# Kernel optimization log

Measured on AMD Instinct MI355X. Metric: run time of the kernel, lower is better.

The kernel has to match this reference:

```python
import jax, jax.numpy as jnp
import numpy as np

B, F_IN, HID, H, S = 256, 1024, 1024, 16, 128
TEMP = float((HID // H) ** 0.5)  # 8.0


def setup_inputs() -> dict:
    key = jax.random.key(0)
    ks = jax.random.split(key, 7)
    return {
        "x": jax.random.normal(ks[0], (B, F_IN, S), dtype=jnp.float32),
        "Wq": jax.random.normal(ks[1], (HID, F_IN), dtype=jnp.float32) * (1.0 / np.sqrt(F_IN)),
        "bq": jax.random.normal(ks[2], (HID,), dtype=jnp.float32) * 0.01,
        "Wk": jax.random.normal(ks[3], (HID, F_IN), dtype=jnp.float32) * (1.0 / np.sqrt(F_IN)),
        "bk": jax.random.normal(ks[4], (HID,), dtype=jnp.float32) * 0.01,
        "Wo": jax.random.normal(ks[5], (S,), dtype=jnp.float32) * (1.0 / np.sqrt(S)),
        "bo": jax.random.normal(ks[6], (1,), dtype=jnp.float32) * 0.01,
    }


def _to_heads(t):
    # (B, F, S) -> (B, H, S, F//H), matching reshape(B,H,F/H,S).permute(0,1,3,2)
    b, f, s = t.shape
    return t.reshape(b, H, f // H, s).transpose(0, 1, 3, 2)


def reference(x, Wq, bq, Wk, bk, Wo, bo):
    # 1x1 Conv1d == per-position linear over channel dim
    q = jnp.einsum('bis,hi->bhs', x, Wq) + bq[None, :, None]
    k = jnp.einsum('bis,hi->bhs', x, Wk) + bk[None, :, None]
    qh = _to_heads(q)          # (B,H,S,HID/H)
    kh = _to_heads(k)          # (B,H,S,HID/H)
    vh = _to_heads(x)          # (B,H,S,F_IN/H)  -- v is the raw input, unprojected
    scores = jnp.einsum('bhsd,bhtd->bhst', qh, kh) / TEMP
    attn = jax.nn.softmax(scores, axis=-1)
    out = jnp.einsum('bhst,bhtd->bhsd', attn, vh)   # (B,H,S,F_IN/H)
    # _reshape_from_batches: (B,H,S,dv) -> (B, F_IN, S)
    out = out.transpose(0, 1, 3, 2).reshape(x.shape[0], F_IN, S)
    # map_o: Linear(num_users, 1) over last axis, then squeeze
    score = jnp.einsum('bfs,s->bf', out, Wo) + bo[0]
    return score
```

## Files before the change

### kernel.cpp

```cpp
#include <hip/hip_runtime.h>

#define F 1024
#define S 128
#define H 16
#define D 64
#define CK 64
#define NCHUNK 16

typedef short bf16x8 __attribute__((ext_vector_type(8)));
typedef float f32x4  __attribute__((ext_vector_type(4)));

#define XS_UNITS ((size_t)128 * NCHUNK * 2048)
#define WB_UNITS ((size_t)8 * NCHUNK * 2048)
#define WS_NEED ((XS_UNITS + WB_UNITS) * 16)

#define MAIN_LDS_BYTES (8192 * 16 + 8 * 128 * 4 + 128 * 4)

__device__ __forceinline__ unsigned short f2bf(float f) {
    unsigned u = __float_as_uint(f);
    u += 0x7fffu + ((u >> 16) & 1u);
    return (unsigned short)(u >> 16);
}

__device__ __forceinline__ uint4 pack8(const float* f) {
    uint4 u;
    u.x = (unsigned)f2bf(f[0]) | ((unsigned)f2bf(f[1]) << 16);
    u.y = (unsigned)f2bf(f[2]) | ((unsigned)f2bf(f[3]) << 16);
    u.z = (unsigned)f2bf(f[4]) | ((unsigned)f2bf(f[5]) << 16);
    u.w = (unsigned)f2bf(f[6]) | ((unsigned)f2bf(f[7]) << 16);
    return u;
}

typedef __attribute__((address_space(1))) const unsigned int as1_u32;
typedef __attribute__((address_space(3))) unsigned int as3_u32;

__device__ __forceinline__ void async_cp16(const uint4* g, uint4* l) {
    __builtin_amdgcn_global_load_lds((as1_u32*)g, (as3_u32*)l, 16, 0, 0);
}

__device__ __forceinline__ void bar()   { asm volatile("s_barrier" ::: "memory"); }
__device__ __forceinline__ void lgkm0() { asm volatile("s_waitcnt lgkmcnt(0)" ::: "memory"); }

template<int N> __device__ __forceinline__ void vmcnt_wait() {
    if constexpr (N == 8)      asm volatile("s_waitcnt vmcnt(8)" ::: "memory");
    else if constexpr (N == 4) asm volatile("s_waitcnt vmcnt(4)" ::: "memory");
    else                       asm volatile("s_waitcnt vmcnt(0)" ::: "memory");
}

__global__ void prep(const float* __restrict__ x,
                     const float* __restrict__ Wq,
                     const float* __restrict__ Wk,
                     uint4* __restrict__ xs,
                     uint4* __restrict__ wb)
{
    __shared__ float tile[64 * 129];
    const int tid = threadIdx.x;
    const int blk = blockIdx.x;
    if (blk < 4096) {
        const int b = blk >> 4, ch = blk & 15;
        const float4* src = (const float4*)(x + ((size_t)b * F + ch * CK) * S);
        float4 v[8];
#pragma unroll
        for (int j = 0; j < 8; ++j) v[j] = src[tid + j * 256];
#pragma unroll
        for (int j = 0; j < 8; ++j) {
            const int e4 = tid + j * 256;
            const int i  = e4 >> 5;
            const int sc = (e4 & 31) * 4;
            tile[i * 129 + sc + 0] = v[j].x;
            tile[i * 129 + sc + 1] = v[j].y;
            tile[i * 129 + sc + 2] = v[j].z;
            tile[i * 129 + sc + 3] = v[j].w;
        }
        __syncthreads();
        uint4* dst = xs + ((size_t)(b >> 1) * NCHUNK + ch) * 2048 + (b & 1) * 128;
#pragma unroll
        for (int j = 0; j < 4; ++j) {
            const int u  = tid + j * 256;
            const int kc = u >> 7;
            const int s  = u & 127;
            float f[8];
#pragma unroll
            for (int jj = 0; jj < 8; ++jj) f[jj] = tile[(kc * 8 + jj) * 129 + s];
            dst[kc * 256 + s] = pack8(f);
        }
    } else {
        const int blk2 = blk - 4096;
        const int h = blk2 >> 4, ch = blk2 & 15;
        uint4* dst = wb + ((size_t)(h >> 1) * NCHUNK + ch) * 2048 + (h & 1) * 128;
#pragma unroll
        for (int j = 0; j < 4; ++j) {
            const int u  = tid + j * 256;
            const int kc = u >> 7;
            const int m  = u & 127;
            const float* srcp = (m < 64)
                ? (Wq + (size_t)(h * D + m) * F + ch * CK + kc * 8)
                : (Wk + (size_t)(h * D + m - 64) * F + ch * CK + kc * 8);
            float f[8];
            float4 a = ((const float4*)srcp)[0];
            float4 c = ((const float4*)srcp)[1];
            f[0] = a.x; f[1] = a.y; f[2] = a.z; f[3] = a.w;
            f[4] = c.x; f[5] = c.y; f[6] = c.z; f[7] = c.w;
            dst[kc * 256 + m] = pack8(f);
        }
    }
}

__device__ __forceinline__ void read4(const uint4* mat, int base, bf16x8 (&r)[4]) {
    r[0] = *(const bf16x8*)&mat[base];
    r[1] = *(const bf16x8*)&mat[base + 16];
    r[2] = *(const bf16x8*)&mat[base + 32];
    r[3] = *(const bf16x8*)&mat[base + 48];
}

template<int RB>
__device__ __forceinline__ void mfma16(f32x4 (&acc)[8][4], const bf16x8 (&af)[4], const bf16x8 (&br)[4]) {
#pragma unroll
    for (int mt = 0; mt < 4; ++mt)
#pragma unroll
        for (int nt = 0; nt < 4; ++nt)
            acc[RB + mt][nt] = __builtin_amdgcn_mfma_f32_16x16x32_bf16(af[mt], br[nt], acc[RB + mt][nt], 0, 0, 0);
}

template<int HALF>
__device__ __forceinline__ void stage_half(uint4* mat, const uint4* wbase, const uint4* xbase,
                                           int tgt, int wv, int lane) {
    const int bufb = (tgt & 1) * 4096;
    const uint4* g;
    int l;
    if constexpr (HALF == 0)      { g = wbase + (size_t)tgt * 2048;        l = bufb;        }
    else if constexpr (HALF == 1) { g = xbase + (size_t)tgt * 2048;        l = bufb + 2048; }
    else if constexpr (HALF == 2) { g = wbase + (size_t)tgt * 2048 + 1024; l = bufb + 1024; }
    else                          { g = xbase + (size_t)tgt * 2048 + 1024; l = bufb + 3072; }
    async_cp16(g + wv * 128 + lane,      &mat[l + wv * 128]);
    async_cp16(g + wv * 128 + 64 + lane, &mat[l + wv * 128 + 64]);
}

template<int CUR, bool I1, bool I2, int W1, int W2, bool DW2>
__device__ __forceinline__ void ktile(uint4* mat, const uint4* wbase, const uint4* xbase,
                                      int t, int wv, int lane, int wm, int wn, int q, int l15,
                                      f32x4 (&acc)[8][4])
{
    bf16x8 af[4], br[4];
    const int abase = CUR * 4096 + wm * 128 + l15;
    const int bbase = CUR * 4096 + 2048 + wn * 64 + l15;
    const int kq = q * 256;
    read4(mat, abase + kq, af);
    read4(mat, bbase + kq, br);
    if constexpr (I1) stage_half<2>(mat, wbase, xbase, t + 1, wv, lane);
    bar(); lgkm0();
    __builtin_amdgcn_s_setprio(1); mfma16<0>(acc, af, br); __builtin_amdgcn_s_setprio(0);
    bar();
    read4(mat, abase + kq + 64, af);
    if constexpr (I1) stage_half<3>(mat, wbase, xbase, t + 1, wv, lane);
    bar(); lgkm0();
    __builtin_amdgcn_s_setprio(1); mfma16<4>(acc, af, br); __builtin_amdgcn_s_setprio(0);
    vmcnt_wait<W1>(); bar();
    read4(mat, abase + kq + 1024, af);
    read4(mat, bbase + kq + 1024, br);
    if constexpr (I2) stage_half<0>(mat, wbase, xbase, t + 2, wv, lane);
    bar(); lgkm0();
    __builtin_amdgcn_s_setprio(1); mfma16<0>(acc, af, br); __builtin_amdgcn_s_setprio(0);
    bar();
    read4(mat, abase + kq + 1024 + 64, af);
    if constexpr (I2) stage_half<1>(mat, wbase, xbase, t + 2, wv, lane);
    bar(); lgkm0();
    __builtin_amdgcn_s_setprio(1); mfma16<4>(acc, af, br); __builtin_amdgcn_s_setprio(0);
    if constexpr (DW2) { vmcnt_wait<W2>(); bar(); }
}

__launch_bounds__(512, 2)
__global__ void attn_main(const float* __restrict__ x,
                          const uint4* __restrict__ xs,
                          const uint4* __restrict__ wb,
                          const float* __restrict__ bq,
                          const float* __restrict__ bk,
                          const float* __restrict__ Wo,
                          const float* __restrict__ bo,
                          float* __restrict__ out)
{
    extern __shared__ char smraw[];
    uint4* mat   = (uint4*)smraw;
    float* wpart = (float*)(smraw + 8192 * 16);
    float* wfin  = wpart + 8 * 128;

    const int tid  = threadIdx.x;
    const int lane = tid & 63;
    const int wv   = tid >> 6;
    const int l15  = lane & 15;
    const int q    = lane >> 4;
    const int wm   = wv >> 2;
    const int wn   = wv & 3;

    const int g    = blockIdx.x;
    const int xcd  = g & 7;
    const int slot = g >> 3;
    const int bg   = xcd * 16 + (slot & 15);
    const int hg   = slot >> 4;

    const uint4* wbase = wb + (size_t)hg * NCHUNK * 2048;
    const uint4* xbase = xs + (size_t)bg * NCHUNK * 2048;

    f32x4 acc[8][4];
#pragma unroll
    for (int mi = 0; mi < 8; ++mi)
#pragma unroll
        for (int ni = 0; ni < 4; ++ni) acc[mi][ni] = (f32x4){0.f, 0.f, 0.f, 0.f};

    stage_half<0>(mat, wbase, xbase, 0, wv, lane);
    stage_half<1>(mat, wbase, xbase, 0, wv, lane);
    stage_half<2>(mat, wbase, xbase, 0, wv, lane);
    stage_half<3>(mat, wbase, xbase, 0, wv, lane);
    stage_half<0>(mat, wbase, xbase, 1, wv, lane);
    stage_half<1>(mat, wbase, xbase, 1, wv, lane);
    vmcnt_wait<8>();
    bar();

#pragma unroll 1
    for (int i = 0; i < 7; ++i) {
        ktile<0, true, true, 8, 8, true>(mat, wbase, xbase, 2 * i,     wv, lane, wm, wn, q, l15, acc);
        ktile<1, true, true, 8, 8, true>(mat, wbase, xbase, 2 * i + 1, wv, lane, wm, wn, q, l15, acc);
    }
    ktile<0, true,  false, 8, 4, true >(mat, wbase, xbase, 14, wv, lane, wm, wn, q, l15, acc);
    ktile<1, false, false, 0, 0, false>(mat, wbase, xbase, 15, wv, lane, wm, wn, q, l15, acc);

    __syncthreads();

    {
        unsigned short* m16 = (unsigned short*)mat;
        const int hglob = hg * 2 + wm;
#pragma unroll
        for (int rt = 0; rt < 8; ++rt) {
            const int mh0   = rt * 16 + q * 4;
            const int d0    = mh0 & 63;
            const int kbase = (mh0 < 64) ? 0 : 1024;
            float bias4[4];
#pragma unroll
            for (int rr = 0; rr < 4; ++rr)
                bias4[rr] = (mh0 < 64) ? bq[hglob * D + d0 + rr] : bk[hglob * D + d0 + rr];
#pragma unroll
            for (int ct = 0; ct < 4; ++ct) {
                const int col = wn * 64 + ct * 16 + l15;
                const int bj  = col >> 7;
                const int s   = col & 127;
                const int c   = wm * 2 + bj;
                unsigned long long pv = 0;
#pragma unroll
                for (int rr = 0; rr < 4; ++rr)
                    pv |= (unsigned long long)f2bf(acc[rt][ct][rr] + bias4[rr]) << (16 * rr);
                const int unit = c * 2048 + kbase + s * 8 + ((d0 >> 3) ^ (s & 7));
                *(unsigned long long*)&m16[unit * 8 + (d0 & 7)] = pv;
            }
        }
    }
    __syncthreads();

    for (int c = 0; c < 4; ++c) {
        const int qb = c * 2048;
        const int kb = c * 2048 + 1024;
        f32x4 p[8];
#pragma unroll
        for (int nt = 0; nt < 8; ++nt) p[nt] = (f32x4){0.f, 0.f, 0.f, 0.f};
#pragma unroll
        for (int ks = 0; ks < 2; ++ks) {
            const int kcq  = ks * 4 + q;
            const int arow = wv * 16 + l15;
            bf16x8 a2 = *(const bf16x8*)&mat[qb + arow * 8 + (kcq ^ (arow & 7))];
            bf16x8 b2[8];
#pragma unroll
            for (int nt = 0; nt < 8; ++nt) {
                const int trow = nt * 16 + l15;
                b2[nt] = *(const bf16x8*)&mat[kb + trow * 8 + (kcq ^ (trow & 7))];
            }
#pragma unroll
            for (int nt = 0; nt < 8; ++nt)
                p[nt] = __builtin_amdgcn_mfma_f32_16x16x32_bf16(a2, b2[nt], p[nt], 0, 0, 0);
        }
        float pw[8];
#pragma unroll
        for (int nt = 0; nt < 8; ++nt) pw[nt] = 0.f;
#pragma unroll
        for (int rr = 0; rr < 4; ++rr) {
            const int srow = wv * 16 + q * 4 + rr;
            float mx = p[0][rr];
#pragma unroll
            for (int nt = 1; nt < 8; ++nt) mx = fmaxf(mx, p[nt][rr]);
#pragma unroll
            for (int off = 1; off < 16; off <<= 1) mx = fmaxf(mx, __shfl_xor(mx, off));
            float e[8];
            float l = 0.f;
#pragma unroll
            for (int nt = 0; nt < 8; ++nt) {
                e[nt] = __expf((p[nt][rr] - mx) * 0.125f);
                l += e[nt];
            }
#pragma unroll
            for (int off = 1; off < 16; off <<= 1) l += __shfl_xor(l, off);
            const float cw = Wo[srow] / l;
#pragma unroll
            for (int nt = 0; nt < 8; ++nt) pw[nt] = fmaf(cw, e[nt], pw[nt]);
        }
#pragma unroll
        for (int nt = 0; nt < 8; ++nt) {
            pw[nt] += __shfl_xor(pw[nt], 16);
            pw[nt] += __shfl_xor(pw[nt], 32);
        }
        if (q == 0) {
#pragma unroll
            for (int nt = 0; nt < 8; ++nt) wpart[wv * 128 + nt * 16 + l15] = pw[nt];
        }
        __syncthreads();
        if (tid < 128) {
            float sum = 0.f;
#pragma unroll
            for (int w = 0; w < 8; ++w) sum += wpart[w * 128 + tid];
            wfin[tid] = sum;
        }
        __syncthreads();
        {
            const int bglob = bg * 2 + (c & 1);
            const int hglob = hg * 2 + (c >> 1);
            const int dd = tid >> 3, part = tid & 7;
            const float4* xv = (const float4*)(x + (size_t)bglob * (F * S)
                                                 + (size_t)(hglob * D + dd) * S + part * 16);
            float a5 = 0.f;
#pragma unroll
            for (int j = 0; j < 4; ++j) {
                float4 vv = xv[j];
                a5 = fmaf(wfin[part * 16 + j * 4 + 0], vv.x, a5);
                a5 = fmaf(wfin[part * 16 + j * 4 + 1], vv.y, a5);
                a5 = fmaf(wfin[part * 16 + j * 4 + 2], vv.z, a5);
                a5 = fmaf(wfin[part * 16 + j * 4 + 3], vv.w, a5);
            }
            a5 += __shfl_xor(a5, 1);
            a5 += __shfl_xor(a5, 2);
            a5 += __shfl_xor(a5, 4);
            if (part == 0) out[(size_t)bglob * F + hglob * D + dd] = a5 + bo[0];
        }
        __syncthreads();
    }
}

struct SmemT {
    uint4 mat[2048];
    float wpart[4][S];
    float wfin[S];
};

__launch_bounds__(256, 4)
__global__ void attn_fallback(const float* __restrict__ x,
                              const float* __restrict__ Wq,
                              const float* __restrict__ bq,
                              const float* __restrict__ Wk,
                              const float* __restrict__ bk,
                              const float* __restrict__ Wo,
                              const float* __restrict__ bo,
                              float* __restrict__ out)
{
    __shared__ SmemT sm;
    const int tid  = threadIdx.x;
    const int lane = tid & 63;
    const int wv   = tid >> 6;
    const int l15  = lane & 15;
    const int q    = lane >> 4;

    const int g    = blockIdx.x;
    const int xcd  = g & 7;
    const int slot = g >> 3;
    const int hg   = slot >> 7;
    const int r0   = slot & 127;
    const int b    = xcd * 32 + (r0 >> 2);
    const int h    = hg * 4 + (r0 & 3);

    const float* xb  = x  + (size_t)b * (F * S);
    const float* wqh = Wq + (size_t)h * D * F;
    const float* wkh = Wk + (size_t)h * D * F;

    const int m0 = (wv & 1) * 64;
    const int n0 = (wv >> 1) * 64;

    f32x4 acc[4][4];
#pragma unroll
    for (int mt = 0; mt < 4; ++mt)
#pragma unroll
        for (int nt = 0; nt < 4; ++nt) acc[mt][nt] = (f32x4){0.f, 0.f, 0.f, 0.f};

    const int mq  = tid >> 2;
    const int kq  = tid & 3;
    const int s0x = (tid & 63) * 2;
    const int iq  = tid >> 6;

    for (int ch = 0; ch < NCHUNK; ++ch) {
        const int c0 = ch * CK;
        __syncthreads();
        {
            const int key = mq & 7;
            float f[16];
            const float4* srcq = (const float4*)(wqh + (size_t)mq * F + (c0 + kq * 16));
#pragma unroll
            for (int j = 0; j < 4; ++j) {
                float4 v = srcq[j];
                f[4*j] = v.x; f[4*j+1] = v.y; f[4*j+2] = v.z; f[4*j+3] = v.w;
            }
            sm.mat[mq * 8 + ((kq * 2    ) ^ key)] = pack8(f);
            sm.mat[mq * 8 + ((kq * 2 + 1) ^ key)] = pack8(f + 8);
            const float4* srck = (const float4*)(wkh + (size_t)mq * F + (c0 + kq * 16));
#pragma unroll
            for (int j = 0; j < 4; ++j) {
                float4 v = srck[j];
                f[4*j] = v.x; f[4*j+1] = v.y; f[4*j+2] = v.z; f[4*j+3] = v.w;
            }
            sm.mat[(64 + mq) * 8 + ((kq * 2    ) ^ key)] = pack8(f);
            sm.mat[(64 + mq) * 8 + ((kq * 2 + 1) ^ key)] = pack8(f + 8);
        }
        {
            const float* src = xb + (size_t)(c0 + iq * 16) * S + s0x;
            float fa[8], fb[8];
#pragma unroll
            for (int grp = 0; grp < 2; ++grp) {
#pragma unroll
                for (int j = 0; j < 8; ++j) {
                    float2 v = *(const float2*)(src + (size_t)(grp * 8 + j) * S);
                    fa[j] = v.x; fb[j] = v.y;
                }
                const int kc = iq * 2 + grp;
                sm.mat[1024 + (s0x    ) * 8 + (kc ^ ((s0x    ) & 7))] = pack8(fa);
                sm.mat[1024 + (s0x + 1) * 8 + (kc ^ ((s0x + 1) & 7))] = pack8(fb);
            }
        }
        __syncthreads();
#pragma unroll
        for (int ks = 0; ks < 2; ++ks) {
            bf16x8 af[4], br[4];
#pragma unroll
            for (int mt = 0; mt < 4; ++mt) {
                const int row = m0 + mt * 16 + l15;
                af[mt] = *(const bf16x8*)&sm.mat[row * 8 + ((ks * 4 + q) ^ (row & 7))];
            }
#pragma unroll
            for (int nt = 0; nt < 4; ++nt) {
                const int row = n0 + nt * 16 + l15;
                br[nt] = *(const bf16x8*)&sm.mat[1024 + row * 8 + ((ks * 4 + q) ^ (row & 7))];
            }
#pragma unroll
            for (int mt = 0; mt < 4; ++mt)
#pragma unroll
                for (int nt = 0; nt < 4; ++nt)
                    acc[mt][nt] = __builtin_amdgcn_mfma_f32_16x16x32_bf16(
                        af[mt], br[nt], acc[mt][nt], 0, 0, 0);
        }
    }

    __syncthreads();
    {
        unsigned short* m16 = (unsigned short*)sm.mat;
#pragma unroll
        for (int mt = 0; mt < 4; ++mt) {
#pragma unroll
            for (int rr = 0; rr < 4; ++rr) {
                const int m = m0 + mt * 16 + q * 4 + rr;
                const int d = m & 63;
                const float bias = (m < 64) ? bq[h * D + d] : bk[h * D + d];
                const int base = (m < 64) ? 0 : 8192;
#pragma unroll
                for (int nt = 0; nt < 4; ++nt) {
                    const int s = n0 + nt * 16 + l15;
                    const float v = acc[mt][nt][rr] + bias;
                    const int unit = s * 8 + (((d >> 3)) ^ (s & 7));
                    m16[base + unit * 8 + (d & 7)] = f2bf(v);
                }
            }
        }
    }
    __syncthreads();

    f32x4 p[2][8];
#pragma unroll
    for (int mt = 0; mt < 2; ++mt)
#pragma unroll
        for (int nt = 0; nt < 8; ++nt) p[mt][nt] = (f32x4){0.f, 0.f, 0.f, 0.f};

#pragma unroll
    for (int ks = 0; ks < 2; ++ks) {
        bf16x8 a2[2], b2[8];
#pragma unroll
        for (int mt = 0; mt < 2; ++mt) {
            const int row = wv * 32 + mt * 16 + l15;
            a2[mt] = *(const bf16x8*)&sm.mat[row * 8 + ((ks * 4 + q) ^ (row & 7))];
        }
#pragma unroll
        for (int nt = 0; nt < 8; ++nt) {
            const int row = nt * 16 + l15;
            b2[nt] = *(const bf16x8*)&sm.mat[1024 + row * 8 + ((ks * 4 + q) ^ (row & 7))];
        }
#pragma unroll
        for (int mt = 0; mt < 2; ++mt)
#pragma unroll
            for (int nt = 0; nt < 8; ++nt)
                p[mt][nt] = __builtin_amdgcn_mfma_f32_16x16x32_bf16(a2[mt], b2[nt], p[mt][nt], 0, 0, 0);
    }

    float pw[8];
#pragma unroll
    for (int nt = 0; nt < 8; ++nt) pw[nt] = 0.f;

#pragma unroll
    for (int mt = 0; mt < 2; ++mt) {
#pragma unroll
        for (int rr = 0; rr < 4; ++rr) {
            const int srow = wv * 32 + mt * 16 + q * 4 + rr;
            float mx = p[mt][0][rr];
#pragma unroll
            for (int nt = 1; nt < 8; ++nt) mx = fmaxf(mx, p[mt][nt][rr]);
#pragma unroll
            for (int off = 1; off < 16; off <<= 1) mx = fmaxf(mx, __shfl_xor(mx, off));
            float e[8];
            float l = 0.f;
#pragma unroll
            for (int nt = 0; nt < 8; ++nt) {
                e[nt] = __expf((p[mt][nt][rr] - mx) * 0.125f);
                l += e[nt];
            }
#pragma unroll
            for (int off = 1; off < 16; off <<= 1) l += __shfl_xor(l, off);
            const float c = Wo[srow] / l;
#pragma unroll
            for (int nt = 0; nt < 8; ++nt) pw[nt] = fmaf(c, e[nt], pw[nt]);
        }
    }
#pragma unroll
    for (int nt = 0; nt < 8; ++nt) {
        pw[nt] += __shfl_xor(pw[nt], 16);
        pw[nt] += __shfl_xor(pw[nt], 32);
    }
    if (q == 0) {
#pragma unroll
        for (int nt = 0; nt < 8; ++nt) sm.wpart[wv][nt * 16 + l15] = pw[nt];
    }
    __syncthreads();
    if (tid < S)
        sm.wfin[tid] = sm.wpart[0][tid] + sm.wpart[1][tid] + sm.wpart[2][tid] + sm.wpart[3][tid];
    __syncthreads();

    {
        const int dd   = tid >> 2;
        const int part = tid & 3;
        const float* xv = xb + (size_t)(h * D + dd) * S + part * 32;
        float a5 = 0.f;
#pragma unroll 8
        for (int t = 0; t < 32; ++t) a5 = fmaf(sm.wfin[part * 32 + t], xv[t], a5);
        a5 += __shfl_xor(a5, 1);
        a5 += __shfl_xor(a5, 2);
        if (part == 0) out[(size_t)b * F + h * D + dd] = a5 + bo[0];
    }
}

extern "C" void kernel_launch(void* const* d_in, const int* in_sizes, int n_in,
                              void* d_out, int out_size, void* d_ws, size_t ws_size,
                              hipStream_t stream) {
    const float* x  = (const float*)d_in[0];
    const float* Wq = (const float*)d_in[1];
    const float* bq = (const float*)d_in[2];
    const float* Wk = (const float*)d_in[3];
    const float* bk = (const float*)d_in[4];
    const float* Wo = (const float*)d_in[5];
    const float* bo = (const float*)d_in[6];
    float* out = (float*)d_out;

    if (ws_size >= WS_NEED) {
        uint4* xsp = (uint4*)d_ws;
        uint4* wbp = (uint4*)((char*)d_ws + XS_UNITS * 16);
        static bool attr_done = false;
        if (!attr_done) {
            (void)hipFuncSetAttribute(reinterpret_cast<const void*>(attn_main),
                                      hipFuncAttributeMaxDynamicSharedMemorySize, MAIN_LDS_BYTES);
            attr_done = true;
        }
        prep<<<dim3(4096 + 256), dim3(256), 0, stream>>>(x, Wq, Wk, xsp, wbp);
        attn_main<<<dim3(1024), dim3(512), MAIN_LDS_BYTES, stream>>>(x, xsp, wbp, bq, bk, Wo, bo, out);
    } else {
        attn_fallback<<<dim3(256 * H), dim3(256), 0, stream>>>(x, Wq, bq, Wk, bk, Wo, bo, out);
    }
}
```

Measured before the change: 372.1 us.

## Read bf16 staged x for value reduction, add sched barriers, vectorize prep transpose

The final attention-times-value reduction now reads V from the bf16 staged copy xs, prefetched before the softmax, instead of reloading fp32 x after the barriers. This halves the bytes of that load and hides its latency behind the softmax work, at the cost of bf16 rounding on V and scattered 2-byte loads. The prep kernel writes its transpose tile as float4 with a padded stride. The main loop replaces inline-asm barriers with builtins and adds sched_barrier fences to pin instruction order.

```diff
diff --git a/kernel.cpp b/kernel.cpp
--- a/kernel.cpp
+++ b/kernel.cpp
@@ -20,6 +20,10 @@
     unsigned u = __float_as_uint(f);
     u += 0x7fffu + ((u >> 16) & 1u);
     return (unsigned short)(u >> 16);
+}
+
+__device__ __forceinline__ float bf2f(unsigned short h) {
+    return __uint_as_float((unsigned)h << 16);
 }
 
 __device__ __forceinline__ uint4 pack8(const float* f) {
@@ -38,13 +42,12 @@
     __builtin_amdgcn_global_load_lds((as1_u32*)g, (as3_u32*)l, 16, 0, 0);
 }
 
-__device__ __forceinline__ void bar()   { asm volatile("s_barrier" ::: "memory"); }
-__device__ __forceinline__ void lgkm0() { asm volatile("s_waitcnt lgkmcnt(0)" ::: "memory"); }
-
-template<int N> __device__ __forceinline__ void vmcnt_wait() {
-    if constexpr (N == 8)      asm volatile("s_waitcnt vmcnt(8)" ::: "memory");
-    else if constexpr (N == 4) asm volatile("s_waitcnt vmcnt(4)" ::: "memory");
-    else                       asm volatile("s_waitcnt vmcnt(0)" ::: "memory");
+__device__ __forceinline__ void bar()   { __builtin_amdgcn_s_barrier(); }
+__device__ __forceinline__ void sb0()   { __builtin_amdgcn_sched_barrier(0); }
+__device__ __forceinline__ void lgkm0() { asm volatile("s_waitcnt lgkmcnt(0)"); }
+
+template<int N> __device__ __forceinline__ void vmw() {
+    asm volatile("s_waitcnt vmcnt(%0)" :: "n"(N));
 }
 
 __global__ void prep(const float* __restrict__ x,
@@ -53,7 +56,7 @@
                      uint4* __restrict__ xs,
                      uint4* __restrict__ wb)
 {
-    __shared__ float tile[64 * 129];
+    __shared__ float4 t4[64 * 33];
     const int tid = threadIdx.x;
     const int blk = blockIdx.x;
     if (blk < 4096) {
@@ -65,14 +68,10 @@
 #pragma unroll
         for (int j = 0; j < 8; ++j) {
             const int e4 = tid + j * 256;
-            const int i  = e4 >> 5;
-            const int sc = (e4 & 31) * 4;
-            tile[i * 129 + sc + 0] = v[j].x;
-            tile[i * 129 + sc + 1] = v[j].y;
-            tile[i * 129 + sc + 2] = v[j].z;
-            tile[i * 129 + sc + 3] = v[j].w;
+            t4[(e4 >> 5) * 33 + (e4 & 31)] = v[j];
         }
         __syncthreads();
+        const float* tile = (const float*)t4;
         uint4* dst = xs + ((size_t)(b >> 1) * NCHUNK + ch) * 2048 + (b & 1) * 128;
 #pragma unroll
         for (int j = 0; j < 4; ++j) {
@@ -81,7 +80,7 @@
             const int s  = u & 127;
             float f[8];
 #pragma unroll
-            for (int jj = 0; jj < 8; ++jj) f[jj] = tile[(kc * 8 + jj) * 129 + s];
+            for (int jj = 0; jj < 8; ++jj) f[jj] = tile[(kc * 8 + jj) * 132 + s];
             dst[kc * 256 + s] = pack8(f);
         }
     } else {
@@ -148,25 +147,25 @@
     read4(mat, abase + kq, af);
     read4(mat, bbase + kq, br);
     if constexpr (I1) stage_half<2>(mat, wbase, xbase, t + 1, wv, lane);
-    bar(); lgkm0();
+    bar(); lgkm0(); sb0();
     __builtin_amdgcn_s_setprio(1); mfma16<0>(acc, af, br); __builtin_amdgcn_s_setprio(0);
-    bar();
+    bar(); sb0();
     read4(mat, abase + kq + 64, af);
     if constexpr (I1) stage_half<3>(mat, wbase, xbase, t + 1, wv, lane);
-    bar(); lgkm0();
+    bar(); lgkm0(); sb0();
     __builtin_amdgcn_s_setprio(1); mfma16<4>(acc, af, br); __builtin_amdgcn_s_setprio(0);
-    vmcnt_wait<W1>(); bar();
+    vmw<W1>(); bar(); sb0();
     read4(mat, abase + kq + 1024, af);
     read4(mat, bbase + kq + 1024, br);
     if constexpr (I2) stage_half<0>(mat, wbase, xbase, t + 2, wv, lane);
-    bar(); lgkm0();
+    bar(); lgkm0(); sb0();
     __builtin_amdgcn_s_setprio(1); mfma16<0>(acc, af, br); __builtin_amdgcn_s_setprio(0);
-    bar();
+    bar(); sb0();
     read4(mat, abase + kq + 1024 + 64, af);
     if constexpr (I2) stage_half<1>(mat, wbase, xbase, t + 2, wv, lane);
-    bar(); lgkm0();
+    bar(); lgkm0(); sb0();
     __builtin_amdgcn_s_setprio(1); mfma16<4>(acc, af, br); __builtin_amdgcn_s_setprio(0);
-    if constexpr (DW2) { vmcnt_wait<W2>(); bar(); }
+    if constexpr (DW2) { vmw<W2>(); bar(); sb0(); }
 }
 
 __launch_bounds__(512, 2)
@@ -179,6 +178,7 @@
                           const float* __restrict__ bo,
                           float* __restrict__ out)
 {
+    (void)x;
     extern __shared__ char smraw[];
     uint4* mat   = (uint4*)smraw;
     float* wpart = (float*)(smraw + 8192 * 16);
@@ -213,8 +213,8 @@
     stage_half<3>(mat, wbase, xbase, 0, wv, lane);
     stage_half<0>(mat, wbase, xbase, 1, wv, lane);
     stage_half<1>(mat, wbase, xbase, 1, wv, lane);
-    vmcnt_wait<8>();
-    bar();
+    vmw<8>();
+    bar(); sb0();
 
 #pragma unroll 1
     for (int i = 0; i < 7; ++i) {
@@ -258,6 +258,9 @@
     for (int c = 0; c < 4; ++c) {
         const int qb = c * 2048;
         const int kb = c * 2048 + 1024;
+        const int bglob = bg * 2 + (c & 1);
+        const int hglob = hg * 2 + (c >> 1);
+
         f32x4 p[8];
 #pragma unroll
         for (int nt = 0; nt < 8; ++nt) p[nt] = (f32x4){0.f, 0.f, 0.f, 0.f};
@@ -276,6 +279,14 @@
             for (int nt = 0; nt < 8; ++nt)
                 p[nt] = __builtin_amdgcn_mfma_f32_16x16x32_bf16(a2, b2[nt], p[nt], 0, 0, 0);
         }
+
+        const int dd = tid >> 3, part = tid & 7;
+        const unsigned short* xp = (const unsigned short*)(xbase + (size_t)hglob * 2048);
+        const int hw0 = ((dd >> 3) * 256 + (bglob & 1) * 128) * 8 + (dd & 7);
+        unsigned short xr[16];
+#pragma unroll
+        for (int jj = 0; jj < 16; ++jj) xr[jj] = xp[hw0 + (part * 16 + jj) * 8];
+
         float pw[8];
 #pragma unroll
         for (int nt = 0; nt < 8; ++nt) pw[nt] = 0.f;
@@ -318,20 +329,10 @@
         }
         __syncthreads();
         {
-            const int bglob = bg * 2 + (c & 1);
-            const int hglob = hg * 2 + (c >> 1);
-            const int dd = tid >> 3, part = tid & 7;
-            const float4* xv = (const float4*)(x + (size_t)bglob * (F * S)
-                                                 + (size_t)(hglob * D + dd) * S + part * 16);
             float a5 = 0.f;
 #pragma unroll
-            for (int j = 0; j < 4; ++j) {
-                float4 vv = xv[j];
-                a5 = fmaf(wfin[part * 16 + j * 4 + 0], vv.x, a5);
-                a5 = fmaf(wfin[part * 16 + j * 4 + 1], vv.y, a5);
-                a5 = fmaf(wfin[part * 16 + j * 4 + 2], vv.z, a5);
-                a5 = fmaf(wfin[part * 16 + j * 4 + 3], vv.w, a5);
-            }
+            for (int jj = 0; jj < 16; ++jj)
+                a5 = fmaf(wfin[part * 16 + jj], bf2f(xr[jj]), a5);
             a5 += __shfl_xor(a5, 1);
             a5 += __shfl_xor(a5, 2);
             a5 += __shfl_xor(a5, 4);
```

Result: no change. 378.0 us (+1.6%).
